# Optimization experiments

Hardware: AMD Instinct MI355X
Metric: run time of the kernel (lower is better)

The kernel has to match this reference:

```python
import jax, jax.numpy as jnp
import numpy as np

HID = 128
FEAT = 16            # glob_in//(2+n_history) = (node_in-1)//4 = (edge_in-1)//4
N_GRAPHS = 512
N_NODES = 100000
N_EDGES = 400000
N_PER = 100000       # effects per branch (glob/node/edge)
A_TOTAL = 300000     # G.num_effects.sum()
EFF_PER_ACT = 4
NUM_ACTIONS = A_TOTAL // EFF_PER_ACT  # 75000 segments (static for jit)


def _lin(k, fan_in, fan_out):
    kw, kb = jax.random.split(k)
    s = 1.0 / np.sqrt(fan_in)
    W = jax.random.uniform(kw, (fan_in, fan_out), jnp.float32, -s, s)
    b = jax.random.uniform(kb, (fan_out,), jnp.float32, -s, s)
    return W, b


def setup_inputs() -> dict:
    key = jax.random.key(0)
    ks = jax.random.split(key, 16)
    globs = jax.random.normal(ks[0], (N_GRAPHS, HID), jnp.float32)
    nodes = jax.random.normal(ks[1], (N_NODES, HID), jnp.float32)
    edges = jax.random.normal(ks[2], (N_EDGES, HID), jnp.float32)
    action_globs = jax.random.normal(ks[3], (N_PER, FEAT), jnp.float32)
    action_nodes = jax.random.normal(ks[4], (N_PER, FEAT), jnp.float32)
    action_edges = jax.random.normal(ks[5], (N_PER, FEAT), jnp.float32)
    row = jax.random.randint(ks[6], (N_EDGES,), 0, N_NODES, jnp.int32)
    col = jax.random.randint(ks[7], (N_EDGES,), 0, N_NODES, jnp.int32)
    U = jax.random.randint(ks[8], (N_PER,), 0, N_GRAPHS, jnp.int32)
    V = jax.random.randint(ks[9], (N_PER,), 0, N_NODES, jnp.int32)
    E = jax.random.randint(ks[10], (N_PER,), 0, N_EDGES, jnp.int32)
    # disjoint write slots in the preallocated actions tensor
    UA = jnp.arange(N_PER, dtype=jnp.int32)
    VA = N_PER + jnp.arange(N_PER, dtype=jnp.int32)
    EA = 2 * N_PER + jnp.arange(N_PER, dtype=jnp.int32)
    # sorted per-effect action ids (4 effects per action)
    actions_batch = (jnp.arange(A_TOTAL, dtype=jnp.int32) // EFF_PER_ACT).astype(jnp.int32)
    glob_W, glob_b = _lin(ks[11], HID + FEAT, HID)
    node_W, node_b = _lin(ks[12], HID + FEAT, HID)
    e1_W, e1_b = _lin(ks[13], 2 * HID + FEAT, HID)
    e2_W, e2_b = _lin(ks[14], 2 * HID, HID)
    pol_W, pol_b = _lin(ks[15], HID, 1)
    return {
        "globs": globs, "nodes": nodes, "edges": edges,
        "action_globs": action_globs, "action_nodes": action_nodes, "action_edges": action_edges,
        "glob_W": glob_W, "glob_b": glob_b, "node_W": node_W, "node_b": node_b,
        "e1_W": e1_W, "e1_b": e1_b, "e2_W": e2_W, "e2_b": e2_b,
        "pol_W": pol_W, "pol_b": pol_b,
        "row": row, "col": col, "U": U, "UA": UA, "V": V, "VA": VA,
        "E": E, "EA": EA, "actions_batch": actions_batch,
    }


def _norm(batch):
    # torch norm(): consecutive group ids starting at batch[0]
    changed = (batch[1:] != batch[:-1]).astype(batch.dtype)
    return batch[0] + jnp.concatenate([jnp.zeros((1,), batch.dtype), jnp.cumsum(changed)])


def reference(globs, nodes, edges, action_globs, action_nodes, action_edges,
              glob_W, glob_b, node_W, node_b, e1_W, e1_b, e2_W, e2_b,
              pol_W, pol_b, row, col, U, UA, V, VA, E, EA, actions_batch):
    actions = jnp.zeros((A_TOTAL, HID), globs.dtype)
    # glob branch: gather globs -> small Linear -> index_put
    ga = jnp.concatenate([globs[U], action_globs], axis=1) @ glob_W + glob_b
    actions = actions.at[UA].set(ga)
    # node branch
    na = jnp.concatenate([nodes[V], action_nodes], axis=1) @ node_W + node_b
    actions = actions.at[VA].set(na)
    # edge branch: two chained Linears over gathered endpoint node feats
    EE = jnp.concatenate([nodes[row[E]], action_edges, nodes[col[E]]], axis=1) @ e1_W + e1_b
    ea = jnp.concatenate([edges[E], EE], axis=1) @ e2_W + e2_b
    actions = actions.at[EA].set(ea)
    # scatter_add segment reduction over action ids
    seg = _norm(actions_batch)
    agg = jax.ops.segment_sum(actions, seg, num_segments=NUM_ACTIONS)  # [NUM_ACTIONS, HID]
    return agg @ pol_W + pol_b  # [NUM_ACTIONS, 1]
```

## Files before the change

kernel.cpp:

```cpp
#include <hip/hip_runtime.h>

#define HID 128
#define FEAT 16
#define N_PER 100000
#define NUM_ACTIONS 75000
#define N_NODES 100000
#define N_GRAPHS 512

#define NSCAL_OFF 1024
#define GSCAL_OFF (NSCAL_OFF + 4 * N_NODES)

__device__ __forceinline__ float dot4(float4 a, float4 b) {
    return a.x * b.x + a.y * b.y + a.z * b.z + a.w * b.w;
}

template <int CTRL>
__device__ __forceinline__ float dpp_mov(float x) {
    return __int_as_float(__builtin_amdgcn_update_dpp(
        0, __float_as_int(x), CTRL, 0xF, 0xF, true));
}
__device__ __forceinline__ float red16(float x) {
    x += dpp_mov<0x111>(x);
    x += dpp_mov<0x112>(x);
    x += dpp_mov<0x114>(x);
    x += dpp_mov<0x118>(x);
    return x;
}
__device__ __forceinline__ float red32(float x) {
    x = red16(x);
    x += dpp_mov<0x142>(x);
    return x;
}
__device__ __forceinline__ float red64(float x) {
    x = red32(x);
    x += dpp_mov<0x143>(x);
    return x;
}

__global__ __launch_bounds__(1024) void fold_kernel(
    const float* __restrict__ glob_W, const float* __restrict__ glob_b,
    const float* __restrict__ node_W, const float* __restrict__ node_b,
    const float* __restrict__ e1_W,  const float* __restrict__ e1_b,
    const float* __restrict__ e2_W,  const float* __restrict__ e2_b,
    const float* __restrict__ pol_W, const float* __restrict__ pol_b,
    float* __restrict__ ws)
{
    __shared__ float qEE[HID];
    const int t = threadIdx.x, wave = t >> 6, lane = t & 63;
    const int bid = blockIdx.x;

    const bool needq = (bid >= 26 && bid <= 43);
    if (needq) {
        const int hw = t >> 5, s = t & 31;
        const float4 p4 = *(const float4*)&pol_W[4 * s];
        #pragma unroll
        for (int r = 0; r < 4; ++r) {
            const int k = hw + 32 * r;
            const float4 x = *(const float4*)&e2_W[(HID + k) * HID + 4 * s];
            float acc = red32(dot4(x, p4));
            if (s == 31) qEE[k] = acc;
        }
        __syncthreads();
    }

    const float2 p2 = *(const float2*)&pol_W[2 * lane];
    const int d = bid * 16 + wave;
    if (d == 691) {
        if (lane == 0) ws[691] = pol_b[0];
    } else if (d < 692) {
        float acc;
        if (d < 144) {
            const float2 x = *(const float2*)&glob_W[d * HID + 2 * lane];
            acc = x.x * p2.x + x.y * p2.y;
        } else if (d < 288) {
            const float2 x = *(const float2*)&node_W[(d - 144) * HID + 2 * lane];
            acc = x.x * p2.x + x.y * p2.y;
        } else if (d < 416) {
            const float2 x = *(const float2*)&e2_W[(d - 288) * HID + 2 * lane];
            acc = x.x * p2.x + x.y * p2.y;
        } else if (d < 688) {
            const float2 q2 = *(const float2*)&qEE[2 * lane];
            const float2 x  = *(const float2*)&e1_W[(d - 416) * HID + 2 * lane];
            acc = x.x * q2.x + x.y * q2.y;
        } else if (d == 688) {
            const float2 x = *(const float2*)&glob_b[2 * lane];
            acc = x.x * p2.x + x.y * p2.y;
        } else if (d == 689) {
            const float2 x = *(const float2*)&node_b[2 * lane];
            acc = x.x * p2.x + x.y * p2.y;
        } else {
            const float2 q2 = *(const float2*)&qEE[2 * lane];
            const float2 x1 = *(const float2*)&e1_b[2 * lane];
            const float2 x2 = *(const float2*)&e2_b[2 * lane];
            acc = x1.x * q2.x + x1.y * q2.y + x2.x * p2.x + x2.y * p2.y;
        }
        acc = red64(acc);
        if (lane == 63) ws[d] = acc;
    }
}

__global__ __launch_bounds__(256) void precompute_kernel(
    const float* __restrict__ nodes, const float* __restrict__ globs,
    float* __restrict__ ws)
{
    const int t = threadIdx.x, s = t & 31;
    const int h = blockIdx.x * 8 + (t >> 5);
    if (h < N_NODES) {
        const float4 fr = *(const float4*)&ws[416 + 4 * s];
        const float4 fc = *(const float4*)&ws[560 + 4 * s];
        const float4 fn = *(const float4*)&ws[144 + 4 * s];
        const float4 x  = *(const float4*)&nodes[h * HID + 4 * s];
        const float ar = red32(dot4(x, fr));
        const float ac = red32(dot4(x, fc));
        const float az = red32(dot4(x, fn));
        if (s == 31) *(float4*)&ws[NSCAL_OFF + 4 * h] = make_float4(ar, ac, az, 0.f);
    } else if (h < N_NODES + N_GRAPHS) {
        const int u = h - N_NODES;
        const float4 fg = *(const float4*)&ws[4 * s];
        const float4 x  = *(const float4*)&globs[u * HID + 4 * s];
        const float a = red32(dot4(x, fg));
        if (s == 31) ws[GSCAL_OFF + u] = a;
    }
}

__global__ __launch_bounds__(256) void actions_kernel(
    const float* __restrict__ edges,
    const float* __restrict__ ag, const float* __restrict__ an,
    const float* __restrict__ ae,
    const int* __restrict__ row, const int* __restrict__ col,
    const int* __restrict__ U, const int* __restrict__ V,
    const int* __restrict__ E,
    const float* __restrict__ ws, float* __restrict__ out)
{
    const int b    = blockIdx.x;
    const int wave = threadIdx.x >> 6;
    const int lane = threadIdx.x & 63;

    if (wave < 2) {
        const bool isg = (wave == 0);
        const int qtr = lane >> 4, ql = lane & 15;
        const int al  = 4 * b + qtr;
        const int gl  = 4 * al;
        const float* feats = isg ? ag : an;
        const int* idx     = isg ? U : V;
        const int wbase    = isg ? 0 : 144;

        float p = 0.f;
        if ((ql & 3) == 0) {
            const int id = idx[gl + (ql >> 2)];
            p = isg ? ws[GSCAL_OFF + id] : ws[NSCAL_OFF + 4 * id + 2];
        }
        const float4 f  = *(const float4*)&feats[gl * FEAT + 4 * ql];
        const float4 wf = *(const float4*)&ws[wbase + HID + 4 * (ql & 3)];
        p = red16(p + dot4(f, wf));
        if (ql == 15)
            out[(isg ? 0 : 25000) + al] = p + 4.f * ws[isg ? 688 : 689] + ws[691];
    } else {
        const int j = b + 6250 * (wave - 2);
        const int s = lane & 31;
        const int al = 2 * j + (lane >> 5);
        const int gl = 4 * al;

        const int4 e4 = *(const int4*)&E[gl];
        const int e[4] = { e4.x, e4.y, e4.z, e4.w };
        float p = 0.f;
        if (s < 8) {
            const int ei = e[s & 3];
            const int id = (s < 4) ? row[ei] : col[ei];
            p = ws[NSCAL_OFF + 4 * id + ((s < 4) ? 0 : 1)];
        }

        const float4 we = *(const float4*)&ws[288 + 4 * s];
        #pragma unroll
        for (int i = 0; i < 4; ++i) {
            const float4 x = *(const float4*)&edges[e[i] * HID + 4 * s];
            p += dot4(x, we);
        }
        if (s < 16) {
            const float4 f  = *(const float4*)&ae[gl * FEAT + 4 * s];
            const float4 wf = *(const float4*)&ws[544 + 4 * (s & 3)];
            p += dot4(f, wf);
        }
        p = red32(p);
        if (s == 31) out[50000 + al] = p + 4.f * ws[690] + ws[691];
    }
}

extern "C" void kernel_launch(void* const* d_in, const int* in_sizes, int n_in,
                              void* d_out, int out_size, void* d_ws, size_t ws_size,
                              hipStream_t stream)
{
    const float* globs  = (const float*)d_in[0];
    const float* nodes  = (const float*)d_in[1];
    const float* edges  = (const float*)d_in[2];
    const float* ag     = (const float*)d_in[3];
    const float* an     = (const float*)d_in[4];
    const float* ae     = (const float*)d_in[5];
    const float* glob_W = (const float*)d_in[6];
    const float* glob_b = (const float*)d_in[7];
    const float* node_W = (const float*)d_in[8];
    const float* node_b = (const float*)d_in[9];
    const float* e1_W   = (const float*)d_in[10];
    const float* e1_b   = (const float*)d_in[11];
    const float* e2_W   = (const float*)d_in[12];
    const float* e2_b   = (const float*)d_in[13];
    const float* pol_W  = (const float*)d_in[14];
    const float* pol_b  = (const float*)d_in[15];
    const int*   row    = (const int*)d_in[16];
    const int*   col    = (const int*)d_in[17];
    const int*   U      = (const int*)d_in[18];
    const int*   V      = (const int*)d_in[20];
    const int*   E      = (const int*)d_in[22];

    float* ws  = (float*)d_ws;
    float* out = (float*)d_out;

    hipLaunchKernelGGL(fold_kernel, dim3(44), dim3(1024), 0, stream,
                       glob_W, glob_b, node_W, node_b, e1_W, e1_b, e2_W, e2_b,
                       pol_W, pol_b, ws);
    hipLaunchKernelGGL(precompute_kernel, dim3((N_NODES + N_GRAPHS + 7) / 8), dim3(256),
                       0, stream, nodes, globs, ws);
    hipLaunchKernelGGL(actions_kernel, dim3(6250), dim3(256), 0, stream,
                       edges, ag, an, ae, row, col, U, V, E, ws, out);
}
```

Before: 37.10 us.

## Fuse weight folding with node/edge scalar precompute into one persistent prep kernel

Merges the weight-folding and per-node precompute kernels into one persistent kernel with 256 blocks of 1024 threads. Each block recomputes the folded weight vectors it needs into shared memory, so no separate fold launch or grid-wide dependency is required. The gathered edge-row dot products move from the actions kernel into the prep kernel, with a prefetch of the next E index. The actions kernel becomes a uniform 16-lanes-per-action reduction over scalars. This saves a launch and its dependency, at the cost of redundant weight folding in every block and fewer, longer-running blocks for the streaming work.

```diff
diff --git a/kernel.cpp b/kernel.cpp
--- a/kernel.cpp
+++ b/kernel.cpp
@@ -9,6 +9,11 @@
 
 #define NSCAL_OFF 1024
 #define GSCAL_OFF (NSCAL_OFF + 4 * N_NODES)
+#define ESCAL_OFF (GSCAL_OFF + N_GRAPHS)
+
+#define NODE_BLOCKS 116
+#define EDGE_BLOCKS 140
+#define PREP_BLOCKS (NODE_BLOCKS + EDGE_BLOCKS)
 
 __device__ __forceinline__ float dot4(float4 a, float4 b) {
     return a.x * b.x + a.y * b.y + a.z * b.z + a.w * b.w;
@@ -31,100 +36,132 @@
     x += dpp_mov<0x142>(x);
     return x;
 }
-__device__ __forceinline__ float red64(float x) {
-    x = red32(x);
-    x += dpp_mov<0x143>(x);
-    return x;
-}
-
-__global__ __launch_bounds__(1024) void fold_kernel(
+
+__global__ __launch_bounds__(1024) void prep_kernel(
+    const float* __restrict__ nodes, const float* __restrict__ globs,
+    const float* __restrict__ edges,
     const float* __restrict__ glob_W, const float* __restrict__ glob_b,
     const float* __restrict__ node_W, const float* __restrict__ node_b,
     const float* __restrict__ e1_W,  const float* __restrict__ e1_b,
     const float* __restrict__ e2_W,  const float* __restrict__ e2_b,
     const float* __restrict__ pol_W, const float* __restrict__ pol_b,
-    float* __restrict__ ws)
+    const int* __restrict__ E, float* __restrict__ ws)
 {
     __shared__ float qEE[HID];
-    const int t = threadIdx.x, wave = t >> 6, lane = t & 63;
+    __shared__ float wA[HID];
+    __shared__ float wB[HID];
+    __shared__ float wC[HID];
+    const int t = threadIdx.x, hw = t >> 5, s = t & 31;
     const int bid = blockIdx.x;
-
-    const bool needq = (bid >= 26 && bid <= 43);
-    if (needq) {
-        const int hw = t >> 5, s = t & 31;
-        const float4 p4 = *(const float4*)&pol_W[4 * s];
+    const float4 p4 = *(const float4*)&pol_W[4 * s];
+
+    if (bid < NODE_BLOCKS) {
         #pragma unroll
         for (int r = 0; r < 4; ++r) {
             const int k = hw + 32 * r;
             const float4 x = *(const float4*)&e2_W[(HID + k) * HID + 4 * s];
-            float acc = red32(dot4(x, p4));
+            const float acc = red32(dot4(x, p4));
             if (s == 31) qEE[k] = acc;
         }
         __syncthreads();
+        const float4 q4 = *(const float4*)&qEE[4 * s];
+        for (int r = 0; r < 4; ++r) {
+            const int k = hw + 32 * r;
+            const float4 xn = *(const float4*)&node_W[k * HID + 4 * s];
+            const float an_ = red32(dot4(xn, p4));
+            if (s == 31) wA[k] = an_;
+            const float4 xr = *(const float4*)&e1_W[k * HID + 4 * s];
+            const float ar = red32(dot4(xr, q4));
+            if (s == 31) wB[k] = ar;
+            const float4 xc = *(const float4*)&e1_W[(144 + k) * HID + 4 * s];
+            const float ac = red32(dot4(xc, q4));
+            if (s == 31) wC[k] = ac;
+        }
+        if (bid == 0) {
+            {
+                const int d = hw;
+                const float* rp = (d < 16) ? &glob_W[(HID + d) * HID]
+                                           : &node_W[(HID + (d - 16)) * HID];
+                const float4 x = *(const float4*)&rp[4 * s];
+                const float acc = red32(dot4(x, p4));
+                if (s == 31) ws[d < 16 ? 128 + d : 272 + (d - 16)] = acc;
+            }
+            if (hw < 20) {
+                float acc; int dst;
+                if (hw < 16) {
+                    const float4 x = *(const float4*)&e1_W[(HID + hw) * HID + 4 * s];
+                    acc = dot4(x, q4); dst = 544 + hw;
+                } else if (hw == 16) {
+                    const float4 x = *(const float4*)&glob_b[4 * s];
+                    acc = dot4(x, p4); dst = 688;
+                } else if (hw == 17) {
+                    const float4 x = *(const float4*)&node_b[4 * s];
+                    acc = dot4(x, p4); dst = 689;
+                } else if (hw == 18) {
+                    const float4 x1 = *(const float4*)&e1_b[4 * s];
+                    const float4 x2 = *(const float4*)&e2_b[4 * s];
+                    acc = dot4(x1, q4) + dot4(x2, p4); dst = 690;
+                } else {
+                    acc = 0.f; dst = 691;
+                }
+                acc = red32(acc);
+                if (s == 31) ws[dst] = (dst == 691) ? pol_b[0] : acc;
+            }
+        }
+        __syncthreads();
+        const float4 fn = *(const float4*)&wA[4 * s];
+        const float4 fr = *(const float4*)&wB[4 * s];
+        const float4 fc = *(const float4*)&wC[4 * s];
+        for (int h = bid * 32 + hw; h < N_NODES; h += NODE_BLOCKS * 32) {
+            const float4 x = *(const float4*)&nodes[h * HID + 4 * s];
+            const float ar = red32(dot4(x, fr));
+            const float ac = red32(dot4(x, fc));
+            const float az = red32(dot4(x, fn));
+            if (s == 31)
+                *(float4*)&ws[NSCAL_OFF + 4 * h] = make_float4(ar, ac, az, 0.f);
+        }
+    } else {
+        const int eb = bid - NODE_BLOCKS;
+        #pragma unroll
+        for (int r = 0; r < 4; ++r) {
+            const int k = hw + 32 * r;
+            const float4 x = *(const float4*)&e2_W[k * HID + 4 * s];
+            const float acc = red32(dot4(x, p4));
+            if (s == 31) wA[k] = acc;
+        }
+        if (eb < 16) {
+            #pragma unroll
+            for (int r = 0; r < 4; ++r) {
+                const int k = hw + 32 * r;
+                const float4 x = *(const float4*)&glob_W[k * HID + 4 * s];
+                const float acc = red32(dot4(x, p4));
+                if (s == 31) wB[k] = acc;
+            }
+        }
+        __syncthreads();
+        const float4 q4 = *(const float4*)&wA[4 * s];
+        if (eb < 16) {
+            const float4 g4 = *(const float4*)&wB[4 * s];
+            const int u = eb * 32 + hw;
+            const float4 x = *(const float4*)&globs[u * HID + 4 * s];
+            const float a = red32(dot4(x, g4));
+            if (s == 31) ws[GSCAL_OFF + u] = a;
+        }
+        int g = eb * 32 + hw;
+        const int stride = EDGE_BLOCKS * 32;
+        int e = (g < N_PER) ? E[g] : 0;
+        while (g < N_PER) {
+            const int gn = g + stride;
+            const int en = (gn < N_PER) ? E[gn] : 0;
+            const float4 x = *(const float4*)&edges[e * HID + 4 * s];
+            const float acc = red32(dot4(x, q4));
+            if (s == 31) ws[ESCAL_OFF + g] = acc;
+            g = gn; e = en;
+        }
     }
-
-    const float2 p2 = *(const float2*)&pol_W[2 * lane];
-    const int d = bid * 16 + wave;
-    if (d == 691) {
-        if (lane == 0) ws[691] = pol_b[0];
-    } else if (d < 692) {
-        float acc;
-        if (d < 144) {
-            const float2 x = *(const float2*)&glob_W[d * HID + 2 * lane];
-            acc = x.x * p2.x + x.y * p2.y;
-        } else if (d < 288) {
-            const float2 x = *(const float2*)&node_W[(d - 144) * HID + 2 * lane];
-            acc = x.x * p2.x + x.y * p2.y;
-        } else if (d < 416) {
-            const float2 x = *(const float2*)&e2_W[(d - 288) * HID + 2 * lane];
-            acc = x.x * p2.x + x.y * p2.y;
-        } else if (d < 688) {
-            const float2 q2 = *(const float2*)&qEE[2 * lane];
-            const float2 x  = *(const float2*)&e1_W[(d - 416) * HID + 2 * lane];
-            acc = x.x * q2.x + x.y * q2.y;
-        } else if (d == 688) {
-            const float2 x = *(const float2*)&glob_b[2 * lane];
-            acc = x.x * p2.x + x.y * p2.y;
-        } else if (d == 689) {
-            const float2 x = *(const float2*)&node_b[2 * lane];
-            acc = x.x * p2.x + x.y * p2.y;
-        } else {
-            const float2 q2 = *(const float2*)&qEE[2 * lane];
-            const float2 x1 = *(const float2*)&e1_b[2 * lane];
-            const float2 x2 = *(const float2*)&e2_b[2 * lane];
-            acc = x1.x * q2.x + x1.y * q2.y + x2.x * p2.x + x2.y * p2.y;
-        }
-        acc = red64(acc);
-        if (lane == 63) ws[d] = acc;
-    }
-}
-
-__global__ __launch_bounds__(256) void precompute_kernel(
-    const float* __restrict__ nodes, const float* __restrict__ globs,
-    float* __restrict__ ws)
-{
-    const int t = threadIdx.x, s = t & 31;
-    const int h = blockIdx.x * 8 + (t >> 5);
-    if (h < N_NODES) {
-        const float4 fr = *(const float4*)&ws[416 + 4 * s];
-        const float4 fc = *(const float4*)&ws[560 + 4 * s];
-        const float4 fn = *(const float4*)&ws[144 + 4 * s];
-        const float4 x  = *(const float4*)&nodes[h * HID + 4 * s];
-        const float ar = red32(dot4(x, fr));
-        const float ac = red32(dot4(x, fc));
-        const float az = red32(dot4(x, fn));
-        if (s == 31) *(float4*)&ws[NSCAL_OFF + 4 * h] = make_float4(ar, ac, az, 0.f);
-    } else if (h < N_NODES + N_GRAPHS) {
-        const int u = h - N_NODES;
-        const float4 fg = *(const float4*)&ws[4 * s];
-        const float4 x  = *(const float4*)&globs[u * HID + 4 * s];
-        const float a = red32(dot4(x, fg));
-        if (s == 31) ws[GSCAL_OFF + u] = a;
-    }
 }
 
 __global__ __launch_bounds__(256) void actions_kernel(
-    const float* __restrict__ edges,
     const float* __restrict__ ag, const float* __restrict__ an,
     const float* __restrict__ ae,
     const int* __restrict__ row, const int* __restrict__ col,
@@ -132,57 +169,43 @@
     const int* __restrict__ E,
     const float* __restrict__ ws, float* __restrict__ out)
 {
-    const int b    = blockIdx.x;
-    const int wave = threadIdx.x >> 6;
-    const int lane = threadIdx.x & 63;
-
-    if (wave < 2) {
-        const bool isg = (wave == 0);
-        const int qtr = lane >> 4, ql = lane & 15;
-        const int al  = 4 * b + qtr;
-        const int gl  = 4 * al;
-        const float* feats = isg ? ag : an;
-        const int* idx     = isg ? U : V;
-        const int wbase    = isg ? 0 : 144;
-
-        float p = 0.f;
-        if ((ql & 3) == 0) {
-            const int id = idx[gl + (ql >> 2)];
-            p = isg ? ws[GSCAL_OFF + id] : ws[NSCAL_OFF + 4 * id + 2];
-        }
-        const float4 f  = *(const float4*)&feats[gl * FEAT + 4 * ql];
-        const float4 wf = *(const float4*)&ws[wbase + HID + 4 * (ql & 3)];
-        p = red16(p + dot4(f, wf));
-        if (ql == 15)
-            out[(isg ? 0 : 25000) + al] = p + 4.f * ws[isg ? 688 : 689] + ws[691];
+    const int tid = threadIdx.x;
+    const int qg  = tid >> 4;
+    const int ql  = tid & 15;
+    const int a   = blockIdx.x * 16 + qg;
+    if (a >= NUM_ACTIONS) return;
+
+    float p;
+    if (a < 25000) {
+        const int gl = 4 * a;
+        const float4 f  = *(const float4*)&ag[gl * FEAT + 4 * ql];
+        const float4 wf = *(const float4*)&ws[128 + 4 * (ql & 3)];
+        p = dot4(f, wf);
+        if ((ql & 3) == 0) p += ws[GSCAL_OFF + U[gl + (ql >> 2)]];
+        p = red16(p);
+        if (ql == 15) out[a] = p + 4.f * ws[688] + ws[691];
+    } else if (a < 50000) {
+        const int gl = 4 * (a - 25000);
+        const float4 f  = *(const float4*)&an[gl * FEAT + 4 * ql];
+        const float4 wf = *(const float4*)&ws[272 + 4 * (ql & 3)];
+        p = dot4(f, wf);
+        if ((ql & 3) == 0) p += ws[NSCAL_OFF + 4 * V[gl + (ql >> 2)] + 2];
+        p = red16(p);
+        if (ql == 15) out[a] = p + 4.f * ws[689] + ws[691];
     } else {
-        const int j = b + 6250 * (wave - 2);
-        const int s = lane & 31;
-        const int al = 2 * j + (lane >> 5);
-        const int gl = 4 * al;
-
-        const int4 e4 = *(const int4*)&E[gl];
-        const int e[4] = { e4.x, e4.y, e4.z, e4.w };
-        float p = 0.f;
-        if (s < 8) {
-            const int ei = e[s & 3];
-            const int id = (s < 4) ? row[ei] : col[ei];
-            p = ws[NSCAL_OFF + 4 * id + ((s < 4) ? 0 : 1)];
-        }
-
-        const float4 we = *(const float4*)&ws[288 + 4 * s];
-        #pragma unroll
-        for (int i = 0; i < 4; ++i) {
-            const float4 x = *(const float4*)&edges[e[i] * HID + 4 * s];
-            p += dot4(x, we);
-        }
-        if (s < 16) {
-            const float4 f  = *(const float4*)&ae[gl * FEAT + 4 * s];
-            const float4 wf = *(const float4*)&ws[544 + 4 * (s & 3)];
-            p += dot4(f, wf);
-        }
-        p = red32(p);
-        if (s == 31) out[50000 + al] = p + 4.f * ws[690] + ws[691];
+        const int gl = 4 * (a - 50000);
+        const float4 f  = *(const float4*)&ae[gl * FEAT + 4 * ql];
+        const float4 wf = *(const float4*)&ws[544 + 4 * (ql & 3)];
+        p = dot4(f, wf);
+        if (ql < 8) {
+            const int e  = E[gl + (ql & 3)];
+            const int id = (ql < 4) ? row[e] : col[e];
+            p += ws[NSCAL_OFF + 4 * id + ((ql < 4) ? 0 : 1)];
+        } else if (ql < 12) {
+            p += ws[ESCAL_OFF + gl + (ql - 8)];
+        }
+        p = red16(p);
+        if (ql == 15) out[a] = p + 4.f * ws[690] + ws[691];
     }
 }
 
@@ -215,11 +238,9 @@
     float* ws  = (float*)d_ws;
     float* out = (float*)d_out;
 
-    hipLaunchKernelGGL(fold_kernel, dim3(44), dim3(1024), 0, stream,
-                       glob_W, glob_b, node_W, node_b, e1_W, e1_b, e2_W, e2_b,
-                       pol_W, pol_b, ws);
-    hipLaunchKernelGGL(precompute_kernel, dim3((N_NODES + N_GRAPHS + 7) / 8), dim3(256),
-                       0, stream, nodes, globs, ws);
-    hipLaunchKernelGGL(actions_kernel, dim3(6250), dim3(256), 0, stream,
-                       edges, ag, an, ae, row, col, U, V, E, ws, out);
-}
+    hipLaunchKernelGGL(prep_kernel, dim3(PREP_BLOCKS), dim3(1024), 0, stream,
+                       nodes, globs, edges, glob_W, glob_b, node_W, node_b,
+                       e1_W, e1_b, e2_W, e2_b, pol_W, pol_b, E, ws);
+    hipLaunchKernelGGL(actions_kernel, dim3((NUM_ACTIONS + 15) / 16), dim3(256),
+                       0, stream, ag, an, ae, row, col, U, V, E, ws, out);
+}
```

New measurement: 38.84 us. +4.7%, slower.

## Move edge-feature dot products into persistent precompute kernel, simplify actions kernel

Applied to the files above, without the earlier changes.

The gathered edge-row projection (edges[E]·q) moves out of the latency-bound actions kernel into the precompute kernel. It now runs in parallel with the node-scalar pass as a separate block range, with software-prefetched indices and grid-stride loops over a fixed block count. The actions kernel becomes a uniform 16-lanes-per-action scalar combine over all three branches. This trades an extra workspace write and read of 100k scalars for overlapping the large edge gather with node precompute and dropping the dependent gather chain from the final kernel.

```diff
diff --git a/kernel.cpp b/kernel.cpp
--- a/kernel.cpp
+++ b/kernel.cpp
@@ -9,6 +9,12 @@
 
 #define NSCAL_OFF 1024
 #define GSCAL_OFF (NSCAL_OFF + 4 * N_NODES)
+#define ESCAL_OFF (GSCAL_OFF + N_GRAPHS)
+
+#define NB 896
+#define EB 1120
+#define GB 16
+#define WORK_BLOCKS (NB + EB + GB)
 
 __device__ __forceinline__ float dot4(float4 a, float4 b) {
     return a.x * b.x + a.y * b.y + a.z * b.z + a.w * b.w;
@@ -99,32 +105,52 @@
     }
 }
 
-__global__ __launch_bounds__(256) void precompute_kernel(
+__global__ __launch_bounds__(256) void work_kernel(
     const float* __restrict__ nodes, const float* __restrict__ globs,
+    const float* __restrict__ edges, const int* __restrict__ E,
     float* __restrict__ ws)
 {
-    const int t = threadIdx.x, s = t & 31;
-    const int h = blockIdx.x * 8 + (t >> 5);
-    if (h < N_NODES) {
+    const int t = threadIdx.x, hw = t >> 5, s = t & 31;
+    const int bid = blockIdx.x;
+
+    if (bid < NB) {
         const float4 fr = *(const float4*)&ws[416 + 4 * s];
         const float4 fc = *(const float4*)&ws[560 + 4 * s];
         const float4 fn = *(const float4*)&ws[144 + 4 * s];
-        const float4 x  = *(const float4*)&nodes[h * HID + 4 * s];
-        const float ar = red32(dot4(x, fr));
-        const float ac = red32(dot4(x, fc));
-        const float az = red32(dot4(x, fn));
-        if (s == 31) *(float4*)&ws[NSCAL_OFF + 4 * h] = make_float4(ar, ac, az, 0.f);
-    } else if (h < N_NODES + N_GRAPHS) {
-        const int u = h - N_NODES;
-        const float4 fg = *(const float4*)&ws[4 * s];
-        const float4 x  = *(const float4*)&globs[u * HID + 4 * s];
-        const float a = red32(dot4(x, fg));
-        if (s == 31) ws[GSCAL_OFF + u] = a;
+        for (int h = bid * 8 + hw; h < N_NODES; h += NB * 8) {
+            const float4 x = *(const float4*)&nodes[h * HID + 4 * s];
+            const float ar = red32(dot4(x, fr));
+            const float ac = red32(dot4(x, fc));
+            const float az = red32(dot4(x, fn));
+            if (s == 31)
+                *(float4*)&ws[NSCAL_OFF + 4 * h] = make_float4(ar, ac, az, 0.f);
+        }
+    } else if (bid < NB + EB) {
+        const int eb = bid - NB;
+        const float4 q4 = *(const float4*)&ws[288 + 4 * s];
+        int g = eb * 8 + hw;
+        const int stride = EB * 8;
+        int e = (g < N_PER) ? E[g] : 0;
+        while (g < N_PER) {
+            const int gn = g + stride;
+            const int en = (gn < N_PER) ? E[gn] : 0;
+            const float4 x = *(const float4*)&edges[e * HID + 4 * s];
+            const float acc = red32(dot4(x, q4));
+            if (s == 31) ws[ESCAL_OFF + g] = acc;
+            g = gn; e = en;
+        }
+    } else {
+        const int gb = bid - NB - EB;
+        const float4 g4 = *(const float4*)&ws[4 * s];
+        for (int u = gb * 8 + hw; u < N_GRAPHS; u += GB * 8) {
+            const float4 x = *(const float4*)&globs[u * HID + 4 * s];
+            const float a = red32(dot4(x, g4));
+            if (s == 31) ws[GSCAL_OFF + u] = a;
+        }
     }
 }
 
 __global__ __launch_bounds__(256) void actions_kernel(
-    const float* __restrict__ edges,
     const float* __restrict__ ag, const float* __restrict__ an,
     const float* __restrict__ ae,
     const int* __restrict__ row, const int* __restrict__ col,
@@ -132,57 +158,43 @@
     const int* __restrict__ E,
     const float* __restrict__ ws, float* __restrict__ out)
 {
-    const int b    = blockIdx.x;
-    const int wave = threadIdx.x >> 6;
-    const int lane = threadIdx.x & 63;
-
-    if (wave < 2) {
-        const bool isg = (wave == 0);
-        const int qtr = lane >> 4, ql = lane & 15;
-        const int al  = 4 * b + qtr;
-        const int gl  = 4 * al;
-        const float* feats = isg ? ag : an;
-        const int* idx     = isg ? U : V;
-        const int wbase    = isg ? 0 : 144;
-
-        float p = 0.f;
-        if ((ql & 3) == 0) {
-            const int id = idx[gl + (ql >> 2)];
-            p = isg ? ws[GSCAL_OFF + id] : ws[NSCAL_OFF + 4 * id + 2];
-        }
-        const float4 f  = *(const float4*)&feats[gl * FEAT + 4 * ql];
-        const float4 wf = *(const float4*)&ws[wbase + HID + 4 * (ql & 3)];
-        p = red16(p + dot4(f, wf));
-        if (ql == 15)
-            out[(isg ? 0 : 25000) + al] = p + 4.f * ws[isg ? 688 : 689] + ws[691];
+    const int tid = threadIdx.x;
+    const int qg  = tid >> 4;
+    const int ql  = tid & 15;
+    const int a   = blockIdx.x * 16 + qg;
+    if (a >= NUM_ACTIONS) return;
+
+    float p;
+    if (a < 25000) {
+        const int gl = 4 * a;
+        const float4 f  = *(const float4*)&ag[gl * FEAT + 4 * ql];
+        const float4 wf = *(const float4*)&ws[128 + 4 * (ql & 3)];
+        p = dot4(f, wf);
+        if ((ql & 3) == 0) p += ws[GSCAL_OFF + U[gl + (ql >> 2)]];
+        p = red16(p);
+        if (ql == 15) out[a] = p + 4.f * ws[688] + ws[691];
+    } else if (a < 50000) {
+        const int gl = 4 * (a - 25000);
+        const float4 f  = *(const float4*)&an[gl * FEAT + 4 * ql];
+        const float4 wf = *(const float4*)&ws[272 + 4 * (ql & 3)];
+        p = dot4(f, wf);
+        if ((ql & 3) == 0) p += ws[NSCAL_OFF + 4 * V[gl + (ql >> 2)] + 2];
+        p = red16(p);
+        if (ql == 15) out[a] = p + 4.f * ws[689] + ws[691];
     } else {
-        const int j = b + 6250 * (wave - 2);
-        const int s = lane & 31;
-        const int al = 2 * j + (lane >> 5);
-        const int gl = 4 * al;
-
-        const int4 e4 = *(const int4*)&E[gl];
-        const int e[4] = { e4.x, e4.y, e4.z, e4.w };
-        float p = 0.f;
-        if (s < 8) {
-            const int ei = e[s & 3];
-            const int id = (s < 4) ? row[ei] : col[ei];
-            p = ws[NSCAL_OFF + 4 * id + ((s < 4) ? 0 : 1)];
-        }
-
-        const float4 we = *(const float4*)&ws[288 + 4 * s];
-        #pragma unroll
-        for (int i = 0; i < 4; ++i) {
-            const float4 x = *(const float4*)&edges[e[i] * HID + 4 * s];
-            p += dot4(x, we);
-        }
-        if (s < 16) {
-            const float4 f  = *(const float4*)&ae[gl * FEAT + 4 * s];
-            const float4 wf = *(const float4*)&ws[544 + 4 * (s & 3)];
-            p += dot4(f, wf);
-        }
-        p = red32(p);
-        if (s == 31) out[50000 + al] = p + 4.f * ws[690] + ws[691];
+        const int gl = 4 * (a - 50000);
+        const float4 f  = *(const float4*)&ae[gl * FEAT + 4 * ql];
+        const float4 wf = *(const float4*)&ws[544 + 4 * (ql & 3)];
+        p = dot4(f, wf);
+        if (ql < 8) {
+            const int e  = E[gl + (ql & 3)];
+            const int id = (ql < 4) ? row[e] : col[e];
+            p += ws[NSCAL_OFF + 4 * id + ((ql < 4) ? 0 : 1)];
+        } else if (ql < 12) {
+            p += ws[ESCAL_OFF + gl + (ql - 8)];
+        }
+        p = red16(p);
+        if (ql == 15) out[a] = p + 4.f * ws[690] + ws[691];
     }
 }
 
@@ -218,8 +230,8 @@
     hipLaunchKernelGGL(fold_kernel, dim3(44), dim3(1024), 0, stream,
                        glob_W, glob_b, node_W, node_b, e1_W, e1_b, e2_W, e2_b,
                        pol_W, pol_b, ws);
-    hipLaunchKernelGGL(precompute_kernel, dim3((N_NODES + N_GRAPHS + 7) / 8), dim3(256),
-                       0, stream, nodes, globs, ws);
-    hipLaunchKernelGGL(actions_kernel, dim3(6250), dim3(256), 0, stream,
-                       edges, ag, an, ae, row, col, U, V, E, ws, out);
-}
+    hipLaunchKernelGGL(work_kernel, dim3(WORK_BLOCKS), dim3(256), 0, stream,
+                       nodes, globs, edges, E, ws);
+    hipLaunchKernelGGL(actions_kernel, dim3((NUM_ACTIONS + 15) / 16), dim3(256),
+                       0, stream, ag, an, ae, row, col, U, V, E, ws, out);
+}
```

Result: faster. 36.12 us (-2.7%).
